# Kernel tuning notes

Hardware: AMD Instinct MI355X
Metric: run time of the kernel (lower is better)

## Reference

```python
import jax, jax.numpy as jnp
import numpy as np

N, C, I, E = 2048, 128, 9, 10   # nodes, channels, num_ell (0e+1o+2e -> 1+3+5), elements
K3, K2, K1 = 23, 8, 3           # CG path counts per correlation order (synthetic)
D0, D1 = 1, 3                   # output irrep dims: 0e, 1o


def setup_inputs() -> dict:
    rng = np.random.default_rng(0)
    f = lambda *s: jnp.asarray(rng.standard_normal(s).astype(np.float32))
    elem = rng.integers(0, E, size=N)
    node_attrs = jnp.asarray(np.eye(E, dtype=np.float32)[elem])  # one-hot element types
    return {
        "node_feats": f(N, C, I),
        "sc": 0.1 * f(N, C * (D0 + D1)),
        "node_attrs": node_attrs,
        # generalized CG U-matrices per output irrep and correlation order (buffers)
        "U3_0": 0.1 * f(D0, I, I, I, K3), "U2_0": 0.1 * f(D0, I, I, K2), "U1_0": 0.1 * f(D0, I, K1),
        "W3_0": 0.1 * f(E, K3, C), "W2_0": 0.1 * f(E, K2, C), "W1_0": 0.1 * f(E, K1, C),
        "U3_1": 0.1 * f(D1, I, I, I, K3), "U2_1": 0.1 * f(D1, I, I, K2), "U1_1": 0.1 * f(D1, I, K1),
        "W3_1": 0.1 * f(E, K3, C), "W2_1": 0.1 * f(E, K2, C), "W1_1": 0.1 * f(E, K1, C),
        # equivariant Linear weights (one [mul_in, mul_out] block per output irrep)
        "Wlin0": f(C, C), "Wlin1": f(C, C),
    }


def _sym_contract(x, y, U3, U2, U1, W3, W2, W1):
    """MACE Contraction for one output irrep (correlation=3).
    x: [N,C,I] node features; y: [N,E] one-hot element attrs.
    Mirrors equations '...ik,ekc,bci,be->bc...', '...k,ekc,be->bc...', 'bc...i,bci->bc...'.
    """
    out = jnp.einsum("dpqik,ekc,nci,ne->ncdpq", U3, W3, x, y)   # corr-3 main term [N,C,d,I,I]
    out = out + jnp.einsum("dpqk,ekc,ne->ncdpq", U2, W2, y)     # add corr-2 weighting
    out = jnp.einsum("ncdpq,ncq->ncdp", out, x)                 # contract one feature index
    out = out + jnp.einsum("dpk,ekc,ne->ncdp", U1, W1, y)       # add corr-1 weighting
    out = jnp.einsum("ncdp,ncp->ncd", out, x)                   # final contraction -> [N,C,d]
    return out


def reference(node_feats, sc, node_attrs, U3_0, U2_0, U1_0, W3_0, W2_0, W1_0,
              U3_1, U2_1, U1_1, W3_1, W2_1, W1_1, Wlin0, Wlin1):
    n = node_feats.shape[0]
    f0 = _sym_contract(node_feats, node_attrs, U3_0, U2_0, U1_0, W3_0, W2_0, W1_0)  # [N,C,1]
    f1 = _sym_contract(node_feats, node_attrs, U3_1, U2_1, U1_1, W3_1, W2_1, W1_1)  # [N,C,3]
    inv = 1.0 / jnp.sqrt(jnp.asarray(C, node_feats.dtype))  # e3nn Linear fan-in normalization
    y0 = jnp.einsum("nud,uw->nwd", f0, Wlin0) * inv
    y1 = jnp.einsum("nud,uw->nwd", f1, Wlin1) * inv
    out = jnp.concatenate([y0.reshape(n, -1), y1.reshape(n, -1)], axis=-1)  # [N, C*(1+3)]
    return out + sc
```

## Files before the change

kernel.cpp:

```cpp
#include <hip/hip_runtime.h>

namespace {
constexpr int N_ = 2048, C_ = 128, I_ = 9, E_ = 10;
constexpr int NSLAB = 40;
constexpr int M_ = 8;
constexpr int NCHUNK = 64;
constexpr int NT3 = 165;
constexpr int NT2 = 45;

constexpr int O_ORDER = 0;
constexpr int O_BOFF  = N_;
constexpr int O_A     = N_ + 16;
constexpr int S_A     = NSLAB * 12 * C_ * 4;
constexpr int O_B     = O_A + S_A;
constexpr int S_B     = NSLAB * 42 * C_ * 4;
constexpr int O_C     = O_B + S_B;
constexpr int S_C     = NSLAB * 3 * C_ * 4;
constexpr int NB_VPRE = 1160;
constexpr int NB_PREP = NB_VPRE + 8;
}

__device__ __forceinline__ float f4lane(float4 v, int l) {
  return l == 0 ? v.x : l == 1 ? v.y : l == 2 ? v.z : v.w;
}

__global__ __launch_bounds__(256) void prep_kernel(
    const float* __restrict__ attrs,
    const float* __restrict__ U3_0, const float* __restrict__ U2_0, const float* __restrict__ U1_0,
    const float* __restrict__ W3_0, const float* __restrict__ W2_0, const float* __restrict__ W1_0,
    const float* __restrict__ U3_1, const float* __restrict__ U2_1, const float* __restrict__ U1_1,
    const float* __restrict__ W3_1, const float* __restrict__ W2_1, const float* __restrict__ W1_1,
    float* __restrict__ ws_f, int* __restrict__ ws_i) {
  int bid = blockIdx.x;
  int t = threadIdx.x;

  if (bid < NB_VPRE) {
    int xcd = bid & 7, j = bid >> 3;
    int sg = j / 29, xp = j % 29;
    int slab = xcd + 8 * sg;
    int e = slab >> 2, dsel = slab & 3;
    int d = dsel ? dsel - 1 : 0;
    const float* U3 = dsel ? U3_1 : U3_0;
    const float* U2 = dsel ? U2_1 : U2_0;
    const float* U1 = dsel ? U1_1 : U1_0;
    const float* W3 = dsel ? W3_1 : W3_0;
    const float* W2 = dsel ? W2_1 : W2_0;
    const float* W1 = dsel ? W1_1 : W1_0;
    int half = t >> 7, c = t & 127;
    __shared__ float sf[8][23];

    if (xp < 21) {
      if (t < 184) {
        int s8 = t / 23, k = t % 23;
        int tt = 8 * xp + s8;
        float v = 0.f;
        if (tt < NT3) {
          int rem = tt, p = 0;
          for (;;) { int tp = (9 - p) * (10 - p) / 2; if (rem < tp) break; rem -= tp; ++p; }
          int q = p;
          for (;;) { int ln = 9 - q; if (rem < ln) break; rem -= ln; ++q; }
          int i = q + rem;
          auto u3 = [&](int a, int b, int g) {
            return U3[(((d * 9 + a) * 9 + b) * 9 + g) * 23 + k];
          };
          if (p == q && q == i)  v = u3(p, p, p);
          else if (p == q)       v = u3(p, p, i) + u3(p, i, p) + u3(i, p, p);
          else if (q == i)       v = u3(p, q, q) + u3(q, p, q) + u3(q, q, p);
          else                   v = u3(p, q, i) + u3(p, i, q) + u3(q, p, i)
                                   + u3(q, i, p) + u3(i, p, q) + u3(i, q, p);
        }
        sf[s8][k] = v;
      }
      __syncthreads();
      int sidx = 2 * xp + half;
      float acc[4] = {0.f, 0.f, 0.f, 0.f};
      for (int k = 0; k < 23; ++k) {
        float w = W3[(e * 23 + k) * C_ + c];
        #pragma unroll
        for (int l = 0; l < 4; ++l) acc[l] = fmaf(sf[half * 4 + l][k], w, acc[l]);
      }
      ((float4*)(ws_f + O_B))[((size_t)slab * 42 + sidx) * C_ + c] =
          make_float4(acc[0], acc[1], acc[2], acc[3]);
    } else if (xp < 27) {
      if (t < 64) {
        int s8 = t / 8, k = t % 8;
        int jj = 8 * (xp - 21) + s8;
        float v = 0.f;
        if (jj < NT2) {
          int rem = jj, p = 0;
          while (rem >= 9 - p) { rem -= 9 - p; ++p; }
          int q = p + rem;
          auto u2 = [&](int a, int b) { return U2[((d * 9 + a) * 9 + b) * 8 + k]; };
          v = (p == q) ? u2(p, p) : u2(p, q) + u2(q, p);
        }
        sf[s8][k] = v;
      }
      __syncthreads();
      int a = 2 * (xp - 21) + half;
      float acc[4] = {0.f, 0.f, 0.f, 0.f};
      for (int k = 0; k < 8; ++k) {
        float w = W2[(e * 8 + k) * C_ + c];
        #pragma unroll
        for (int l = 0; l < 4; ++l) acc[l] = fmaf(sf[half * 4 + l][k], w, acc[l]);
      }
      ((float4*)(ws_f + O_A))[((size_t)slab * 12 + a) * C_ + c] =
          make_float4(acc[0], acc[1], acc[2], acc[3]);
    } else {
      int ci, p0;
      if (xp == 27) { ci = half; p0 = 4 * half; }
      else { if (half) return; ci = 2; p0 = 8; }
      float acc[4] = {0.f, 0.f, 0.f, 0.f};
      for (int k = 0; k < 3; ++k) {
        float w = W1[(e * 3 + k) * C_ + c];
        #pragma unroll
        for (int l = 0; l < 4; ++l)
          if (p0 + l < 9) acc[l] = fmaf(U1[(d * 9 + p0 + l) * 3 + k], w, acc[l]);
      }
      ((float4*)(ws_f + O_C))[((size_t)slab * 3 + ci) * C_ + c] =
          make_float4(acc[0], acc[1], acc[2], acc[3]);
    }
  } else if (bid == NB_VPRE) {
    __shared__ int cnt[E_], base_s[E_ + 1], cur[E_];
    __shared__ short elem_s[N_];
    if (t < E_) cnt[t] = 0;
    __syncthreads();
    for (int n = t; n < N_; n += 256) {
      const float* a = attrs + n * E_;
      int best = 0; float bv = a[0];
      for (int e = 1; e < E_; ++e) { float v = a[e]; if (v > bv) { bv = v; best = e; } }
      elem_s[n] = (short)best;
      atomicAdd(&cnt[best], 1);
    }
    __syncthreads();
    if (t == 0) {
      int s = 0;
      for (int e = 0; e < E_; ++e) { base_s[e] = s; cur[e] = s; s += cnt[e]; }
      base_s[E_] = s;
    }
    __syncthreads();
    for (int n = t; n < N_; n += 256) {
      int p = atomicAdd(&cur[elem_s[n]], 1);
      ws_i[O_ORDER + p] = n;
    }
    if (t <= E_) ws_i[O_BOFF + t] = base_s[t];
  }
}

__device__ __forceinline__ void accum_all(const float4* __restrict__ A4,
                                          const float4* __restrict__ B4,
                                          const float4* __restrict__ C4,
                                          const float (&xm)[M_][I_], float (&f)[M_]) {
  #pragma unroll
  for (int p = 0; p < 9; ++p) {
    #pragma unroll
    for (int q = p; q < 9; ++q) {
      const int j  = 45 - (9 - p) * (10 - p) / 2 + (q - p);
      const int tb = 165 - (9 - p) * (10 - p) * (11 - p) / 6
                   + (9 - p) * (10 - p) / 2 - (9 - q) * (10 - q) / 2 - q;
      float s2 = f4lane(A4[(j >> 2) * C_], j & 3);
      float tv[M_];
      #pragma unroll
      for (int m = 0; m < M_; ++m) tv[m] = s2;
      #pragma unroll
      for (int i = q; i < 9; ++i) {
        const int tt = tb + i;
        float v = f4lane(B4[(tt >> 2) * C_], tt & 3);
        #pragma unroll
        for (int m = 0; m < M_; ++m) tv[m] = fmaf(xm[m][i], v, tv[m]);
      }
      #pragma unroll
      for (int m = 0; m < M_; ++m)
        f[m] = fmaf(xm[m][p] * xm[m][q], tv[m], f[m]);
    }
  }
  #pragma unroll
  for (int p = 0; p < 9; ++p) {
    float v = f4lane(C4[(p >> 2) * C_], p & 3);
    #pragma unroll
    for (int m = 0; m < M_; ++m) f[m] = fmaf(xm[m][p], v, f[m]);
  }
}

__global__ __launch_bounds__(128, 1) void contract12_kernel(
    const float* __restrict__ x, const float* __restrict__ ws_f,
    const int* __restrict__ ws_i,
    const float* __restrict__ Wlin0, const float* __restrict__ Wlin1,
    const float* __restrict__ sc, float* __restrict__ out) {
  int bid = blockIdx.x;
  int xcd = bid & 7;
  int sg  = (bid >> 3) % 5;
  int chunk = bid / 40;
  int slab = xcd + 8 * sg;
  int e = slab >> 2, dsel = slab & 3;
  int b0 = ws_i[O_BOFF + e];
  int cnt_e = ws_i[O_BOFF + e + 1] - b0;
  int base = chunk * M_;
  if (base >= cnt_e) return;
  int cnt = cnt_e - base; if (cnt > M_) cnt = M_;
  int c = threadIdx.x;

  const float4* A4 = (const float4*)(ws_f + O_A) + (size_t)slab * 12 * C_ + c;
  const float4* B4 = (const float4*)(ws_f + O_B) + (size_t)slab * 42 * C_ + c;
  const float4* C4 = (const float4*)(ws_f + O_C) + (size_t)slab * 3 * C_ + c;

  int nn[M_];
  #pragma unroll
  for (int m = 0; m < M_; ++m) {
    int idx = base + m; if (idx >= cnt_e) idx = cnt_e - 1;
    nn[m] = ws_i[O_ORDER + b0 + idx];
  }
  float xm[M_][I_];
  #pragma unroll
  for (int m = 0; m < M_; ++m) {
    const float* xp = x + ((size_t)nn[m] * C_ + c) * I_;
    #pragma unroll
    for (int i = 0; i < I_; ++i) xm[m][i] = xp[i];
  }
  float f[M_];
  #pragma unroll
  for (int m = 0; m < M_; ++m) f[m] = 0.f;

  accum_all(A4, B4, C4, xm, f);

  __shared__ float fs[M_][C_ + 1];
  #pragma unroll
  for (int m = 0; m < M_; ++m) fs[m][c] = f[m];
  __syncthreads();

  const float* Wl = (dsel == 0) ? Wlin0 : Wlin1;
  float acc[M_];
  #pragma unroll
  for (int m = 0; m < M_; ++m) acc[m] = 0.f;
  for (int u = 0; u < C_; ++u) {
    float wv = Wl[u * C_ + c];
    #pragma unroll
    for (int m = 0; m < M_; ++m) acc[m] = fmaf(fs[m][u], wv, acc[m]);
  }
  constexpr float inv = 0.08838834764831843f;
  int col = (dsel == 0) ? c : C_ + c * 3 + (dsel - 1);
  #pragma unroll
  for (int m = 0; m < M_; ++m) {
    if (m < cnt) {
      int o = nn[m] * 512 + col;
      out[o] = acc[m] * inv + sc[o];
    }
  }
}

extern "C" void kernel_launch(void* const* d_in, const int* in_sizes, int n_in,
                              void* d_out, int out_size, void* d_ws, size_t ws_size,
                              hipStream_t stream) {
  const float* node_feats = (const float*)d_in[0];
  const float* sc         = (const float*)d_in[1];
  const float* node_attrs = (const float*)d_in[2];
  const float* U3_0 = (const float*)d_in[3];
  const float* U2_0 = (const float*)d_in[4];
  const float* U1_0 = (const float*)d_in[5];
  const float* W3_0 = (const float*)d_in[6];
  const float* W2_0 = (const float*)d_in[7];
  const float* W1_0 = (const float*)d_in[8];
  const float* U3_1 = (const float*)d_in[9];
  const float* U2_1 = (const float*)d_in[10];
  const float* U1_1 = (const float*)d_in[11];
  const float* W3_1 = (const float*)d_in[12];
  const float* W2_1 = (const float*)d_in[13];
  const float* W1_1 = (const float*)d_in[14];
  const float* Wlin0 = (const float*)d_in[15];
  const float* Wlin1 = (const float*)d_in[16];

  float* ws_f = (float*)d_ws;
  int*   ws_i = (int*)d_ws;

  prep_kernel<<<NB_PREP, 256, 0, stream>>>(
      node_attrs,
      U3_0, U2_0, U1_0, W3_0, W2_0, W1_0,
      U3_1, U2_1, U1_1, W3_1, W2_1, W1_1, ws_f, ws_i);

  contract12_kernel<<<NSLAB * NCHUNK, 128, 0, stream>>>(
      node_feats, ws_f, ws_i, Wlin0, Wlin1, sc, (float*)d_out);
}
```

Baseline: 42.90 us.

## Pre-gather node features into element-sorted channel-major layout and remap blocks per element to XCD

Splits bucketing into its own 1024-thread kernel. The prep kernel now also gathers node features into a workspace buffer, sorted by element and laid out channel-major ([j][i][c]), so the contraction kernel reads them coalesced instead of with stride 9. Block-to-slab mapping changes so all four irrep slabs of one element land on the same XCD, so the gathered x and the precomputed tensors for that element can share that XCD's L2. This adds a third launch and an extra global write/read pass over x. It also drops the launch_bounds min-blocks hint and adds an unroll on the linear loop.

```diff
diff --git a/kernel.cpp b/kernel.cpp
--- a/kernel.cpp
+++ b/kernel.cpp
@@ -2,11 +2,10 @@
 
 namespace {
 constexpr int N_ = 2048, C_ = 128, I_ = 9, E_ = 10;
-constexpr int NSLAB = 40;
 constexpr int M_ = 8;
-constexpr int NCHUNK = 64;
 constexpr int NT3 = 165;
 constexpr int NT2 = 45;
+constexpr int NSLAB = 40;
 
 constexpr int O_ORDER = 0;
 constexpr int O_BOFF  = N_;
@@ -16,29 +15,62 @@
 constexpr int S_B     = NSLAB * 42 * C_ * 4;
 constexpr int O_C     = O_B + S_B;
 constexpr int S_C     = NSLAB * 3 * C_ * 4;
-constexpr int NB_VPRE = 1160;
-constexpr int NB_PREP = NB_VPRE + 8;
+constexpr int O_XG    = O_C + S_C;
+constexpr int NB_VPRE2 = 1856;
+constexpr int NB_PREP2 = NB_VPRE2 + 1024;
+constexpr int NB_CONTRACT = 8 * 2 * 4 * 64;
 }
 
 __device__ __forceinline__ float f4lane(float4 v, int l) {
   return l == 0 ? v.x : l == 1 ? v.y : l == 2 ? v.z : v.w;
 }
 
-__global__ __launch_bounds__(256) void prep_kernel(
-    const float* __restrict__ attrs,
+__global__ __launch_bounds__(1024) void bucket_kernel(const float* __restrict__ attrs,
+                                                      int* __restrict__ ws_i) {
+  __shared__ int cnt[E_], base_s[E_ + 1], cur[E_];
+  __shared__ short elem_s[N_];
+  int t = threadIdx.x;
+  if (t < E_) cnt[t] = 0;
+  __syncthreads();
+  for (int n = t; n < N_; n += 1024) {
+    const float* a = attrs + n * E_;
+    int best = 0; float bv = a[0];
+    for (int e = 1; e < E_; ++e) { float v = a[e]; if (v > bv) { bv = v; best = e; } }
+    elem_s[n] = (short)best;
+    atomicAdd(&cnt[best], 1);
+  }
+  __syncthreads();
+  if (t == 0) {
+    int s = 0;
+    for (int e = 0; e < E_; ++e) { base_s[e] = s; cur[e] = s; s += cnt[e]; }
+    base_s[E_] = s;
+  }
+  __syncthreads();
+  for (int n = t; n < N_; n += 1024) {
+    int p = atomicAdd(&cur[elem_s[n]], 1);
+    ws_i[O_ORDER + p] = n;
+  }
+  if (t <= E_) ws_i[O_BOFF + t] = base_s[t];
+}
+
+__global__ __launch_bounds__(256) void prep2_kernel(
+    const float* __restrict__ x,
     const float* __restrict__ U3_0, const float* __restrict__ U2_0, const float* __restrict__ U1_0,
     const float* __restrict__ W3_0, const float* __restrict__ W2_0, const float* __restrict__ W1_0,
     const float* __restrict__ U3_1, const float* __restrict__ U2_1, const float* __restrict__ U1_1,
     const float* __restrict__ W3_1, const float* __restrict__ W2_1, const float* __restrict__ W1_1,
-    float* __restrict__ ws_f, int* __restrict__ ws_i) {
+    float* __restrict__ ws_f, const int* __restrict__ ws_i) {
   int bid = blockIdx.x;
   int t = threadIdx.x;
 
-  if (bid < NB_VPRE) {
-    int xcd = bid & 7, j = bid >> 3;
-    int sg = j / 29, xp = j % 29;
-    int slab = xcd + 8 * sg;
-    int e = slab >> 2, dsel = slab & 3;
+  if (bid < NB_VPRE2) {
+    int xcd = bid & 7, u = bid >> 3;
+    int sl = u / 29, xp = u % 29;
+    int S = (xcd < 2) ? 8 : 4;
+    if (sl >= S) return;
+    int e = xcd + 8 * (sl >> 2);
+    int dsel = sl & 3;
+    int slab = e * 4 + dsel;
     int d = dsel ? dsel - 1 : 0;
     const float* U3 = dsel ? U3_1 : U3_0;
     const float* U2 = dsel ? U2_1 : U2_0;
@@ -119,30 +151,29 @@
       ((float4*)(ws_f + O_C))[((size_t)slab * 3 + ci) * C_ + c] =
           make_float4(acc[0], acc[1], acc[2], acc[3]);
     }
-  } else if (bid == NB_VPRE) {
-    __shared__ int cnt[E_], base_s[E_ + 1], cur[E_];
-    __shared__ short elem_s[N_];
-    if (t < E_) cnt[t] = 0;
-    __syncthreads();
-    for (int n = t; n < N_; n += 256) {
-      const float* a = attrs + n * E_;
-      int best = 0; float bv = a[0];
-      for (int e = 1; e < E_; ++e) { float v = a[e]; if (v > bv) { bv = v; best = e; } }
-      elem_s[n] = (short)best;
-      atomicAdd(&cnt[best], 1);
+  } else {
+    int b2 = bid - NB_VPRE2;
+    int xcd = b2 & 7;
+    int k = b2 >> 3;
+    int cntA = ws_i[O_BOFF + xcd + 1] - ws_i[O_BOFF + xcd];
+    int cntB = (xcd < 2) ? (ws_i[O_BOFF + xcd + 9] - ws_i[O_BOFF + xcd + 8]) : 0;
+    int tot = cntA + cntB;
+    if (k * 16 >= tot) return;
+    int half = t >> 7, c = t & 127;
+    for (int r = 0; r < 8; ++r) {
+      int jl = k * 16 + r * 2 + half;
+      if (jl >= tot) break;
+      int j = (jl < cntA) ? ws_i[O_BOFF + xcd] + jl
+                          : ws_i[O_BOFF + xcd + 8] + (jl - cntA);
+      int node = ws_i[O_ORDER + j];
+      const float* xp = x + ((size_t)node * C_ + c) * I_;
+      float v[I_];
+      #pragma unroll
+      for (int i = 0; i < I_; ++i) v[i] = xp[i];
+      #pragma unroll
+      for (int i = 0; i < I_; ++i)
+        ws_f[O_XG + ((size_t)j * I_ + i) * C_ + c] = v[i];
     }
-    __syncthreads();
-    if (t == 0) {
-      int s = 0;
-      for (int e = 0; e < E_; ++e) { base_s[e] = s; cur[e] = s; s += cnt[e]; }
-      base_s[E_] = s;
-    }
-    __syncthreads();
-    for (int n = t; n < N_; n += 256) {
-      int p = atomicAdd(&cur[elem_s[n]], 1);
-      ws_i[O_ORDER + p] = n;
-    }
-    if (t <= E_) ws_i[O_BOFF + t] = base_s[t];
   }
 }
 
@@ -181,22 +212,22 @@
   }
 }
 
-__global__ __launch_bounds__(128, 1) void contract12_kernel(
-    const float* __restrict__ x, const float* __restrict__ ws_f,
-    const int* __restrict__ ws_i,
+__global__ __launch_bounds__(128) void contract14_kernel(
+    const float* __restrict__ ws_f, const int* __restrict__ ws_i,
     const float* __restrict__ Wlin0, const float* __restrict__ Wlin1,
     const float* __restrict__ sc, float* __restrict__ out) {
   int bid = blockIdx.x;
   int xcd = bid & 7;
-  int sg  = (bid >> 3) % 5;
-  int chunk = bid / 40;
-  int slab = xcd + 8 * sg;
-  int e = slab >> 2, dsel = slab & 3;
+  int r = bid >> 3;
+  int eg = r & 1, dsel = (r >> 1) & 3, chunk = r >> 3;
+  int e = xcd + 8 * eg;
+  if (e >= E_) return;
   int b0 = ws_i[O_BOFF + e];
   int cnt_e = ws_i[O_BOFF + e + 1] - b0;
   int base = chunk * M_;
   if (base >= cnt_e) return;
   int cnt = cnt_e - base; if (cnt > M_) cnt = M_;
+  int slab = e * 4 + dsel;
   int c = threadIdx.x;
 
   const float4* A4 = (const float4*)(ws_f + O_A) + (size_t)slab * 12 * C_ + c;
@@ -212,9 +243,10 @@
   float xm[M_][I_];
   #pragma unroll
   for (int m = 0; m < M_; ++m) {
-    const float* xp = x + ((size_t)nn[m] * C_ + c) * I_;
+    int idx = base + m; if (idx >= cnt_e) idx = cnt_e - 1;
+    const float* xp = ws_f + O_XG + ((size_t)(b0 + idx) * I_) * C_ + c;
     #pragma unroll
-    for (int i = 0; i < I_; ++i) xm[m][i] = xp[i];
+    for (int i = 0; i < I_; ++i) xm[m][i] = xp[i * C_];
   }
   float f[M_];
   #pragma unroll
@@ -231,6 +263,7 @@
   float acc[M_];
   #pragma unroll
   for (int m = 0; m < M_; ++m) acc[m] = 0.f;
+  #pragma unroll 8
   for (int u = 0; u < C_; ++u) {
     float wv = Wl[u * C_ + c];
     #pragma unroll
@@ -271,11 +304,13 @@
   float* ws_f = (float*)d_ws;
   int*   ws_i = (int*)d_ws;
 
-  prep_kernel<<<NB_PREP, 256, 0, stream>>>(
-      node_attrs,
+  bucket_kernel<<<1, 1024, 0, stream>>>(node_attrs, ws_i);
+
+  prep2_kernel<<<NB_PREP2, 256, 0, stream>>>(
+      node_feats,
       U3_0, U2_0, U1_0, W3_0, W2_0, W1_0,
       U3_1, U2_1, U1_1, W3_1, W2_1, W1_1, ws_f, ws_i);
 
-  contract12_kernel<<<NSLAB * NCHUNK, 128, 0, stream>>>(
-      node_feats, ws_f, ws_i, Wlin0, Wlin1, sc, (float*)d_out);
-}
+  contract14_kernel<<<NB_CONTRACT, 128, 0, stream>>>(
+      ws_f, ws_i, Wlin0, Wlin1, sc, (float*)d_out);
+}
```

New measurement: 49.75 us. 1.16x slower.
